# Kernel optimization log

Hardware: AMD Instinct MI355X
Metric: run time of the kernel (lower is better)

## Reference

```python
import jax, jax.numpy as jnp
import numpy as np

N = 50000      # nodes
R = 4          # relations
EMB = 128      # embedding size
H = 4          # heads
S = EMB // H   # per-head size (32)
E = 400000     # total edges (100k per relation)


def setup_inputs() -> dict:
    key = jax.random.key(0)
    ks = jax.random.split(key, 8)
    def u(k, shape, sc):
        return jax.random.uniform(k, shape, jnp.float32, -sc, sc)
    sS = 1.0 / np.sqrt(S)
    sE = 1.0 / np.sqrt(EMB)
    return {
        "x": jax.random.normal(ks[0], (N, EMB), jnp.float32),
        "tokeys": u(ks[1], (R, H, S, S), sS),
        "toqueries": u(ks[2], (R, H, S, S), sS),
        "tovals": u(ks[3], (R, H, S, S), sS),
        "unify": u(ks[4], (R, EMB, EMB), sE),
        "edge_sub": jax.random.randint(ks[5], (E,), 0, N),
        "edge_pred": jax.random.randint(ks[6], (E,), 0, R),
        "edge_obj": jax.random.randint(ks[7], (E,), 0, N),
    }


def reference(x, tokeys, toqueries, tovals, unify, edge_sub, edge_pred, edge_obj):
    n, e = x.shape
    r, h, s, _ = tokeys.shape
    xh = x.reshape(n, h, s)  # x is broadcast (expanded) across relations in the original

    # per-relation, per-head projections: [r, n, h, s]
    keys = jnp.einsum('rhij,nhj->rnhi', tokeys, xh)
    queries = jnp.einsum('rhij,nhj->rnhi', toqueries, xh)
    values = jnp.einsum('rhij,nhj->rnhi', tovals, xh)

    # gather per edge: key at subject, query at object (as in the torch code)
    skeys = keys[edge_pred, edge_sub]        # [E, h, s]
    squeries = queries[edge_pred, edge_obj]  # [E, h, s]
    dot = jnp.einsum('ehi,ehi->eh', skeys, squeries)  # [E, h]

    # segment softmax over rows of the (n*r, n*r) sparse matrix, per head
    row = edge_sub + edge_pred * n  # [E]
    num_seg = n * r
    seg_max = jax.ops.segment_max(dot, row, num_segments=num_seg)  # [n*r, h]
    ex = jnp.exp(dot - seg_max[row])
    seg_sum = jax.ops.segment_sum(ex, row, num_segments=num_seg)
    att = ex / seg_sum[row]  # [E, h]

    # sparse batched matmul: out[row] += att * values[col]  (util.batchmm)
    vals_g = values[edge_pred, edge_obj]          # [E, h, s]
    msg = att[:, :, None] * vals_g                # [E, h, s]
    agg = jax.ops.segment_sum(msg, row, num_segments=num_seg)  # [n*r, h, s]

    out = agg.reshape(r, n, e).transpose(1, 0, 2)  # [n, r, e] (h*s merged = e)
    out = jnp.einsum('rij,nrj->nri', unify, out)   # per-relation unify matmul
    return jax.nn.relu(out.sum(axis=1))            # SumUnify: relu(sum over relations)
```

## Files before the change

kernel.cpp:

```cpp
#include <hip/hip_runtime.h>

constexpr int N_NODES = 50000;
constexpr int N_REL   = 4;
constexpr int EMBD    = 128;
constexpr int N_HEAD  = 4;
constexpr int HS      = 32;
constexpr int N_EDGE  = 400000;
constexpr int N_ROWS  = N_REL * N_NODES;

typedef __attribute__((ext_vector_type(8))) short bf16x8;
typedef __attribute__((ext_vector_type(4))) float f32x4;
typedef unsigned short ushort_t;
typedef unsigned int   uint_t;

__device__ __forceinline__ ushort_t f2b(float f) {
    unsigned int u = __float_as_uint(f);
    u += 0x7FFF + ((u >> 16) & 1);
    return (ushort_t)(u >> 16);
}
__device__ __forceinline__ float lo_bf(uint_t u) {
    return __uint_as_float(u << 16);
}
__device__ __forceinline__ float hi_bf(uint_t u) {
    return __uint_as_float(u & 0xFFFF0000u);
}

__global__ __launch_bounds__(256) void prep_kernel(
    const float* __restrict__ x,
    const float* __restrict__ tk, const float* __restrict__ tq,
    const float* __restrict__ tv, const float* __restrict__ un,
    ushort_t* __restrict__ XB, int* __restrict__ HIST,
    ushort_t* __restrict__ Ct, ushort_t* __restrict__ Mb)
{
    int idx = blockIdx.x * 256 + threadIdx.x;
    if (idx < N_NODES * EMBD) {
        XB[idx] = f2b(x[idx]);
        if (idx < N_ROWS) HIST[idx] = 0;
    } else {
        int jj = idx - N_NODES * EMBD;
        if (jj < 16384) {
            int a = jj & 31, b = (jj >> 5) & 31, rh = jj >> 10;
            const float* tks = tk + rh * 1024;
            const float* tqs = tq + rh * 1024;
            float acc = 0.f;
            #pragma unroll
            for (int s = 0; s < 32; s++) acc += tks[s * 32 + a] * tqs[s * 32 + b];
            Ct[jj] = f2b(acc);
        } else {
            int j  = jj - 16384;
            int jc = j & 127, i = (j >> 7) & 127, r = j >> 14;
            int h = jc >> 5, k = jc & 31;
            const float* us  = un + ((size_t)(r * 128 + i)) * 128 + h * 32;
            const float* tvs = tv + (r * 4 + h) * 1024 + k;
            float acc = 0.f;
            #pragma unroll
            for (int s = 0; s < 32; s++) acc += us[s] * tvs[s * 32];
            Mb[j] = f2b(acc);
        }
    }
}

__global__ __launch_bounds__(512) void proj_mfma(
    const ushort_t* __restrict__ XB, const ushort_t* __restrict__ Ct,
    ushort_t* __restrict__ KT)
{
    __shared__ ushort_t xs[128 * 136];

    const int t    = threadIdx.x;
    const int lane = t & 63;
    const int w    = t >> 6;
    const int n0   = blockIdx.x * 128;

    {
        const uint4* x4 = (const uint4*)(XB + (size_t)n0 * 128);
        for (int idx = t; idx < 128 * 16; idx += 512) {
            int nn = idx >> 4, c = idx & 15;
            uint4 v = make_uint4(0, 0, 0, 0);
            if (n0 + nn < N_NODES) v = x4[idx];
            *(uint4*)&xs[nn * 136 + c * 8] = v;
        }
    }
    __syncthreads();

    const int row  = lane & 15;
    const int kg   = lane >> 4;
    const int rgrp = lane >> 4;

    #pragma unroll 1
    for (int r = 0; r < N_REL; r++) {
        f32x4 acc[8];
        #pragma unroll
        for (int f = 0; f < 8; f++) {
            const int h = f >> 1;
            bf16x8 a = *(const bf16x8*)&xs[(w * 16 + row) * 136 + h * 32 + kg * 8];
            const ushort_t* bp = Ct + (((r * 4 + h) * 32 + (f & 1) * 16 + row) * 32) + kg * 8;
            bf16x8 b = *(const bf16x8*)bp;
            acc[f] = __builtin_amdgcn_mfma_f32_16x16x32_bf16(
                         a, b, (f32x4){0.f, 0.f, 0.f, 0.f}, 0, 0, 0);
        }
        #pragma unroll
        for (int f = 0; f < 8; f++) {
            #pragma unroll
            for (int reg = 0; reg < 4; reg++) {
                int n = n0 + w * 16 + rgrp * 4 + reg;
                if (n < N_NODES)
                    KT[((size_t)r * N_NODES + n) * 128 + f * 16 + row] = f2b(acc[f][reg]);
            }
        }
    }
}

__global__ __launch_bounds__(256) void hist_kernel(
    const int* __restrict__ esub, const int* __restrict__ epred, int* __restrict__ HIST)
{
    int e = blockIdx.x * 256 + threadIdx.x;
    if (e < N_EDGE) atomicAdd(&HIST[epred[e] * N_NODES + esub[e]], 1);
}

__global__ __launch_bounds__(256) void scan_p1(
    const int* __restrict__ HIST, int* __restrict__ SUMS)
{
    int b = blockIdx.x, t = threadIdx.x;
    int base = b * 1024 + t * 4;
    int s = 0;
    #pragma unroll
    for (int k = 0; k < 4; k++) if (base + k < N_ROWS) s += HIST[base + k];
    __shared__ int red[256];
    red[t] = s; __syncthreads();
    for (int st = 128; st > 0; st >>= 1) {
        if (t < st) red[t] += red[t + st];
        __syncthreads();
    }
    if (t == 0) SUMS[b] = red[0];
}

__global__ __launch_bounds__(256) void scan_p2(
    const int* __restrict__ SUMS, int* __restrict__ SOFF, int* __restrict__ OFFS)
{
    int t = threadIdx.x;
    __shared__ int sh[256];
    int o = (t < 196) ? SUMS[t] : 0;
    sh[t] = o; __syncthreads();
    for (int st = 1; st < 256; st <<= 1) {
        int v = (t >= st) ? sh[t - st] : 0;
        __syncthreads();
        sh[t] += v;
        __syncthreads();
    }
    if (t < 196) SOFF[t] = sh[t] - o;
    if (t == 0)  OFFS[N_ROWS] = sh[255];
}

__global__ __launch_bounds__(256) void scan_p3(
    const int* __restrict__ HIST, const int* __restrict__ SOFF,
    int* __restrict__ OFFS, int* __restrict__ CURSOR)
{
    int b = blockIdx.x, t = threadIdx.x;
    int base = b * 1024 + t * 4;
    int v[4], tot = 0;
    #pragma unroll
    for (int k = 0; k < 4; k++) {
        v[k] = (base + k < N_ROWS) ? HIST[base + k] : 0;
        tot += v[k];
    }
    __shared__ int sh[256];
    sh[t] = tot; __syncthreads();
    for (int st = 1; st < 256; st <<= 1) {
        int q = (t >= st) ? sh[t - st] : 0;
        __syncthreads();
        sh[t] += q;
        __syncthreads();
    }
    int run = SOFF[b] + (sh[t] - tot);
    #pragma unroll
    for (int k = 0; k < 4; k++) {
        if (base + k < N_ROWS) { OFFS[base + k] = run; CURSOR[base + k] = run; run += v[k]; }
    }
}

__global__ __launch_bounds__(256) void scatter_kernel(
    const int* __restrict__ esub, const int* __restrict__ epred, const int* __restrict__ eobj,
    int* __restrict__ CURSOR, int* __restrict__ OBJS)
{
    int e = blockIdx.x * 256 + threadIdx.x;
    if (e < N_EDGE) {
        int row = epred[e] * N_NODES + esub[e];
        int pos = atomicAdd(&CURSOR[row], 1);
        OBJS[pos] = eobj[e];
    }
}

__global__ __launch_bounds__(256) void agg_fused(
    const int* __restrict__ OFFS, const int* __restrict__ OBJS,
    const uint_t* __restrict__ KT64, const uint_t* __restrict__ XB64,
    uint_t* __restrict__ AGG64)
{
    const int t    = threadIdx.x;
    const int lane = t & 63;
    const int row0 = (blockIdx.x * 4 + (t >> 6)) * 4;

    int off[5];
    #pragma unroll
    for (int q = 0; q < 5; q++) off[q] = OFFS[row0 + q];

    float klo[4], khi[4], aclo[4], achi[4], seg[4];
    int   it[4];
    #pragma unroll
    for (int q = 0; q < 4; q++) {
        it[q] = off[q];
        aclo[q] = 0.f; achi[q] = 0.f; seg[q] = 0.f;
        klo[q] = 0.f;  khi[q] = 0.f;
        if (off[q] < off[q + 1]) {
            uint_t ku = KT64[(unsigned)(row0 + q) * 64u + lane];
            klo[q] = lo_bf(ku); khi[q] = hi_bf(ku);
        }
    }

    while (it[0] < off[1] || it[1] < off[2] || it[2] < off[3] || it[3] < off[4]) {
        uint_t xu[4];
        bool   d[4];
        #pragma unroll
        for (int q = 0; q < 4; q++) {
            d[q]  = it[q] < off[q + 1];
            xu[q] = 0;
            if (d[q]) xu[q] = XB64[(unsigned)OBJS[it[q]] * 64u + lane];
        }
        float p[4];
        #pragma unroll
        for (int q = 0; q < 4; q++)
            p[q] = klo[q] * lo_bf(xu[q]) + khi[q] * hi_bf(xu[q]);
        #pragma unroll
        for (int m = 1; m < 16; m <<= 1) {
            #pragma unroll
            for (int q = 0; q < 4; q++) p[q] += __shfl_xor(p[q], m, 64);
        }
        #pragma unroll
        for (int q = 0; q < 4; q++) {
            if (d[q]) {
                float ex = __expf(p[q]);
                aclo[q] += ex * lo_bf(xu[q]);
                achi[q] += ex * hi_bf(xu[q]);
                seg[q]  += ex;
                it[q]++;
            }
        }
    }

    #pragma unroll
    for (int q = 0; q < 4; q++) {
        uint_t o = 0u;
        if (off[q] < off[q + 1]) {
            float inv = 1.0f / seg[q];
            o = (uint_t)f2b(aclo[q] * inv) | ((uint_t)f2b(achi[q] * inv) << 16);
        }
        AGG64[(unsigned)(row0 + q) * 64u + lane] = o;
    }
}

__global__ __launch_bounds__(256) void unify_mfma(
    const ushort_t* __restrict__ AGG,
    const ushort_t* __restrict__ Ub, float* __restrict__ out)
{
    __shared__ ushort_t As[64 * 136];
    __shared__ ushort_t Bs[128 * 136];

    const int t    = threadIdx.x;
    const int lane = t & 63;
    const int w    = t >> 6;
    const int n0   = blockIdx.x * 64;

    f32x4 acc[8];
    #pragma unroll
    for (int f = 0; f < 8; f++) acc[f] = (f32x4){0.f, 0.f, 0.f, 0.f};

    for (int r = 0; r < N_REL; r++) {
        __syncthreads();

        {
            const uint4* a4 = (const uint4*)(AGG + ((size_t)r * N_NODES + n0) * 128);
            for (int idx = t; idx < 64 * 16; idx += 256) {
                int nn = idx >> 4, c = idx & 15;
                uint4 v = make_uint4(0, 0, 0, 0);
                if (n0 + nn < N_NODES) v = a4[idx];
                *(uint4*)&As[nn * 136 + c * 8] = v;
            }
        }
        {
            const uint4* u4 = (const uint4*)(Ub + (size_t)r * 128 * 128);
            for (int idx = t; idx < 128 * 16; idx += 256) {
                int i = idx >> 4, c = idx & 15;
                *(uint4*)&Bs[i * 136 + c * 8] = u4[idx];
            }
        }
        __syncthreads();

        const int row = lane & 15;
        const int kg  = lane >> 4;
        #pragma unroll
        for (int ks = 0; ks < 4; ks++) {
            const int kofs = ks * 32 + kg * 8;
            bf16x8 a = *(const bf16x8*)&As[(w * 16 + row) * 136 + kofs];
            #pragma unroll
            for (int f = 0; f < 8; f++) {
                bf16x8 b = *(const bf16x8*)&Bs[(f * 16 + row) * 136 + kofs];
                acc[f] = __builtin_amdgcn_mfma_f32_16x16x32_bf16(a, b, acc[f], 0, 0, 0);
            }
        }
    }

    const int col  = lane & 15;
    const int rgrp = lane >> 4;
    #pragma unroll
    for (int f = 0; f < 8; f++) {
        #pragma unroll
        for (int reg = 0; reg < 4; reg++) {
            int n = n0 + w * 16 + rgrp * 4 + reg;
            if (n < N_NODES)
                out[(size_t)n * 128 + f * 16 + col] = fmaxf(acc[f][reg], 0.f);
        }
    }
}

extern "C" void kernel_launch(void* const* d_in, const int* in_sizes, int n_in,
                              void* d_out, int out_size, void* d_ws, size_t ws_size,
                              hipStream_t stream)
{
    const float* x  = (const float*)d_in[0];
    const float* tk = (const float*)d_in[1];
    const float* tq = (const float*)d_in[2];
    const float* tv = (const float*)d_in[3];
    const float* un = (const float*)d_in[4];
    const int* esub  = (const int*)d_in[5];
    const int* epred = (const int*)d_in[6];
    const int* eobj  = (const int*)d_in[7];
    float* out = (float*)d_out;

    char* ws = (char*)d_ws;
    ushort_t* KT  = (ushort_t*)(ws);
    ushort_t* XB  = (ushort_t*)(ws + 51200000);
    ushort_t* AGG = (ushort_t*)(ws + 64000000);
    int*      HIST= (int*)     (ws + 115200000);
    int*      SUMS= (int*)     (ws + 116000000);
    int*      SOFF= (int*)     (ws + 116004096);
    int*      OFFS= (int*)     (ws + 116008192);
    int*      OBJS= (int*)     (ws + 116816000);
    ushort_t* Mb  = (ushort_t*)(ws + 118416000);
    ushort_t* Ct  = (ushort_t*)(ws + 118547072);

    prep_kernel<<<(N_NODES * EMBD + 81920) / 256, 256, 0, stream>>>(
        x, tk, tq, tv, un, XB, HIST, Ct, Mb);

    hist_kernel<<<(N_EDGE + 255) / 256, 256, 0, stream>>>(esub, epred, HIST);
    scan_p1<<<196, 256, 0, stream>>>(HIST, SUMS);
    scan_p2<<<1, 256, 0, stream>>>(SUMS, SOFF, OFFS);
    scan_p3<<<196, 256, 0, stream>>>(HIST, SOFF, OFFS, HIST);
    scatter_kernel<<<(N_EDGE + 255) / 256, 256, 0, stream>>>(esub, epred, eobj, HIST, OBJS);

    proj_mfma<<<(N_NODES + 127) / 128, 512, 0, stream>>>(XB, Ct, KT);

    agg_fused<<<N_ROWS / 16, 256, 0, stream>>>(OFFS, OBJS,
                                               (const uint_t*)KT, (const uint_t*)XB,
                                               (uint_t*)AGG);

    unify_mfma<<<(N_NODES + 63) / 64, 256, 0, stream>>>(AGG, Mb, out);
}
```

Measured before the change: 174.1 us.

## Bin rows by degree so aggregation warps process similar-length segments

Adds a degree histogram per scan block, a global bin scan and a scatter that builds a row permutation sorted by (clamped) degree. The aggregation kernel then assigns four degree-similar rows per wavefront via this permutation, reducing divergence where the loop runs to the longest of four rows. Dot-product shuffles are also moved inside the per-row active branch to skip reductions for finished rows. Costs two extra small kernels and indirect, less coalesced row access for K and output writes.

```diff
diff --git a/kernel.cpp b/kernel.cpp
--- a/kernel.cpp
+++ b/kernel.cpp
@@ -7,6 +7,8 @@
 constexpr int HS      = 32;
 constexpr int N_EDGE  = 400000;
 constexpr int N_ROWS  = N_REL * N_NODES;
+constexpr int N_SBLK  = 196;
+constexpr int N_BIN   = 16;
 
 typedef __attribute__((ext_vector_type(8))) short bf16x8;
 typedef __attribute__((ext_vector_type(4))) float f32x4;
@@ -139,7 +141,7 @@
 {
     int t = threadIdx.x;
     __shared__ int sh[256];
-    int o = (t < 196) ? SUMS[t] : 0;
+    int o = (t < N_SBLK) ? SUMS[t] : 0;
     sh[t] = o; __syncthreads();
     for (int st = 1; st < 256; st <<= 1) {
         int v = (t >= st) ? sh[t - st] : 0;
@@ -147,13 +149,13 @@
         sh[t] += v;
         __syncthreads();
     }
-    if (t < 196) SOFF[t] = sh[t] - o;
+    if (t < N_SBLK) SOFF[t] = sh[t] - o;
     if (t == 0)  OFFS[N_ROWS] = sh[255];
 }
 
 __global__ __launch_bounds__(256) void scan_p3(
     const int* __restrict__ HIST, const int* __restrict__ SOFF,
-    int* __restrict__ OFFS, int* __restrict__ CURSOR)
+    int* __restrict__ OFFS, int* __restrict__ CURSOR, int* __restrict__ BH)
 {
     int b = blockIdx.x, t = threadIdx.x;
     int base = b * 1024 + t * 4;
@@ -164,7 +166,13 @@
         tot += v[k];
     }
     __shared__ int sh[256];
+    __shared__ int bh[N_BIN];
+    if (t < N_BIN) bh[t] = 0;
     sh[t] = tot; __syncthreads();
+    #pragma unroll
+    for (int k = 0; k < 4; k++) {
+        if (base + k < N_ROWS) atomicAdd(&bh[min(v[k], 15)], 1);
+    }
     for (int st = 1; st < 256; st <<= 1) {
         int q = (t >= st) ? sh[t - st] : 0;
         __syncthreads();
@@ -176,6 +184,8 @@
     for (int k = 0; k < 4; k++) {
         if (base + k < N_ROWS) { OFFS[base + k] = run; CURSOR[base + k] = run; run += v[k]; }
     }
+    __syncthreads();
+    if (t < N_BIN) BH[b * N_BIN + t] = bh[t];
 }
 
 __global__ __launch_bounds__(256) void scatter_kernel(
@@ -190,54 +200,101 @@
     }
 }
 
+__global__ __launch_bounds__(256) void bin_scan(
+    const int* __restrict__ BH, int* __restrict__ BOFF)
+{
+    constexpr int TOT = N_SBLK * N_BIN;
+    __shared__ int vals[TOT];
+    __shared__ int part[256];
+    int t = threadIdx.x;
+    for (int i = t; i < TOT; i += 256) {
+        int bin = i / N_SBLK, blk = i % N_SBLK;
+        vals[i] = BH[blk * N_BIN + bin];
+    }
+    __syncthreads();
+    int c0 = t * 13;
+    int s = 0;
+    for (int k = 0; k < 13; k++) { int i = c0 + k; if (i < TOT) s += vals[i]; }
+    part[t] = s; __syncthreads();
+    for (int st = 1; st < 256; st <<= 1) {
+        int v = (t >= st) ? part[t - st] : 0;
+        __syncthreads();
+        part[t] += v;
+        __syncthreads();
+    }
+    int run = (t > 0) ? part[t - 1] : 0;
+    for (int k = 0; k < 13; k++) {
+        int i = c0 + k;
+        if (i < TOT) {
+            int bin = i / N_SBLK, blk = i % N_SBLK;
+            int v = vals[i];
+            BOFF[blk * N_BIN + bin] = run;
+            run += v;
+        }
+    }
+}
+
+__global__ __launch_bounds__(256) void bin_scatter(
+    const int* __restrict__ OFFS, const int* __restrict__ BOFF, int* __restrict__ ROWIDX)
+{
+    __shared__ int cur[N_BIN];
+    int b = blockIdx.x, t = threadIdx.x;
+    if (t < N_BIN) cur[t] = BOFF[b * N_BIN + t];
+    __syncthreads();
+    int base = b * 1024 + t * 4;
+    #pragma unroll
+    for (int k = 0; k < 4; k++) {
+        int i = base + k;
+        if (i < N_ROWS) {
+            int deg = OFFS[i + 1] - OFFS[i];
+            int pos = atomicAdd(&cur[min(deg, 15)], 1);
+            ROWIDX[pos] = i;
+        }
+    }
+}
+
 __global__ __launch_bounds__(256) void agg_fused(
-    const int* __restrict__ OFFS, const int* __restrict__ OBJS,
+    const int* __restrict__ ROWIDX, const int* __restrict__ OFFS,
+    const int* __restrict__ OBJS,
     const uint_t* __restrict__ KT64, const uint_t* __restrict__ XB64,
     uint_t* __restrict__ AGG64)
 {
     const int t    = threadIdx.x;
     const int lane = t & 63;
-    const int row0 = (blockIdx.x * 4 + (t >> 6)) * 4;
-
-    int off[5];
-    #pragma unroll
-    for (int q = 0; q < 5; q++) off[q] = OFFS[row0 + q];
-
+    const int s0   = (blockIdx.x * 4 + (t >> 6)) * 4;
+
+    int rows[4], bq[4], eq[4], it[4];
     float klo[4], khi[4], aclo[4], achi[4], seg[4];
-    int   it[4];
     #pragma unroll
     for (int q = 0; q < 4; q++) {
-        it[q] = off[q];
+        rows[q] = ROWIDX[s0 + q];
+        bq[q] = OFFS[rows[q]];
+        eq[q] = OFFS[rows[q] + 1];
+        it[q] = bq[q];
         aclo[q] = 0.f; achi[q] = 0.f; seg[q] = 0.f;
         klo[q] = 0.f;  khi[q] = 0.f;
-        if (off[q] < off[q + 1]) {
-            uint_t ku = KT64[(unsigned)(row0 + q) * 64u + lane];
+        if (bq[q] < eq[q]) {
+            uint_t ku = KT64[(unsigned)rows[q] * 64u + lane];
             klo[q] = lo_bf(ku); khi[q] = hi_bf(ku);
         }
     }
 
-    while (it[0] < off[1] || it[1] < off[2] || it[2] < off[3] || it[3] < off[4]) {
+    while (it[0] < eq[0] || it[1] < eq[1] || it[2] < eq[2] || it[3] < eq[3]) {
         uint_t xu[4];
         bool   d[4];
         #pragma unroll
         for (int q = 0; q < 4; q++) {
-            d[q]  = it[q] < off[q + 1];
+            d[q]  = it[q] < eq[q];
             xu[q] = 0;
             if (d[q]) xu[q] = XB64[(unsigned)OBJS[it[q]] * 64u + lane];
         }
-        float p[4];
-        #pragma unroll
-        for (int q = 0; q < 4; q++)
-            p[q] = klo[q] * lo_bf(xu[q]) + khi[q] * hi_bf(xu[q]);
-        #pragma unroll
-        for (int m = 1; m < 16; m <<= 1) {
-            #pragma unroll
-            for (int q = 0; q < 4; q++) p[q] += __shfl_xor(p[q], m, 64);
-        }
         #pragma unroll
         for (int q = 0; q < 4; q++) {
             if (d[q]) {
-                float ex = __expf(p[q]);
+                float p = klo[q] * lo_bf(xu[q]) + khi[q] * hi_bf(xu[q]);
+                #pragma unroll
+                for (int m = 1; m < 16; m <<= 1) p += __shfl_xor(p, m, 64);
+                float ex = __expf(p);
                 aclo[q] += ex * lo_bf(xu[q]);
                 achi[q] += ex * hi_bf(xu[q]);
                 seg[q]  += ex;
@@ -249,11 +306,11 @@
     #pragma unroll
     for (int q = 0; q < 4; q++) {
         uint_t o = 0u;
-        if (off[q] < off[q + 1]) {
+        if (bq[q] < eq[q]) {
             float inv = 1.0f / seg[q];
             o = (uint_t)f2b(aclo[q] * inv) | ((uint_t)f2b(achi[q] * inv) << 16);
         }
-        AGG64[(unsigned)(row0 + q) * 64u + lane] = o;
+        AGG64[(unsigned)rows[q] * 64u + lane] = o;
     }
 }
 
@@ -336,29 +393,35 @@
     float* out = (float*)d_out;
 
     char* ws = (char*)d_ws;
-    ushort_t* KT  = (ushort_t*)(ws);
-    ushort_t* XB  = (ushort_t*)(ws + 51200000);
-    ushort_t* AGG = (ushort_t*)(ws + 64000000);
-    int*      HIST= (int*)     (ws + 115200000);
-    int*      SUMS= (int*)     (ws + 116000000);
-    int*      SOFF= (int*)     (ws + 116004096);
-    int*      OFFS= (int*)     (ws + 116008192);
-    int*      OBJS= (int*)     (ws + 116816000);
-    ushort_t* Mb  = (ushort_t*)(ws + 118416000);
-    ushort_t* Ct  = (ushort_t*)(ws + 118547072);
+    ushort_t* KT    = (ushort_t*)(ws);
+    ushort_t* XB    = (ushort_t*)(ws + 51200000);
+    ushort_t* AGG   = (ushort_t*)(ws + 64000000);
+    int*      HIST  = (int*)     (ws + 115200000);
+    int*      SUMS  = (int*)     (ws + 116000000);
+    int*      SOFF  = (int*)     (ws + 116004096);
+    int*      OFFS  = (int*)     (ws + 116008192);
+    int*      OBJS  = (int*)     (ws + 116816000);
+    ushort_t* Mb    = (ushort_t*)(ws + 118416000);
+    ushort_t* Ct    = (ushort_t*)(ws + 118547072);
+    int*      ROWIDX= (int*)     (ws + 118579840);
+    int*      BH    = (int*)     (ws + 119379840);
+    int*      BOFF  = (int*)     (ws + 119396224);
 
     prep_kernel<<<(N_NODES * EMBD + 81920) / 256, 256, 0, stream>>>(
         x, tk, tq, tv, un, XB, HIST, Ct, Mb);
 
     hist_kernel<<<(N_EDGE + 255) / 256, 256, 0, stream>>>(esub, epred, HIST);
-    scan_p1<<<196, 256, 0, stream>>>(HIST, SUMS);
+    scan_p1<<<N_SBLK, 256, 0, stream>>>(HIST, SUMS);
     scan_p2<<<1, 256, 0, stream>>>(SUMS, SOFF, OFFS);
-    scan_p3<<<196, 256, 0, stream>>>(HIST, SOFF, OFFS, HIST);
+    scan_p3<<<N_SBLK, 256, 0, stream>>>(HIST, SOFF, OFFS, HIST, BH);
     scatter_kernel<<<(N_EDGE + 255) / 256, 256, 0, stream>>>(esub, epred, eobj, HIST, OBJS);
 
+    bin_scan<<<1, 256, 0, stream>>>(BH, BOFF);
+    bin_scatter<<<N_SBLK, 256, 0, stream>>>(OFFS, BOFF, ROWIDX);
+
     proj_mfma<<<(N_NODES + 127) / 128, 512, 0, stream>>>(XB, Ct, KT);
 
-    agg_fused<<<N_ROWS / 16, 256, 0, stream>>>(OFFS, OBJS,
+    agg_fused<<<N_ROWS / 16, 256, 0, stream>>>(ROWIDX, OFFS, OBJS,
                                                (const uint_t*)KT, (const uint_t*)XB,
                                                (uint_t*)AGG);
 
```

Result: slower. 197.7 us (+13.6%).

## Remap aggregation to half-wave per row with 8-byte loads and two-edge unroll

Applied to the files above, without the earlier changes.

The aggregation kernel now assigns each CSR row to 32 lanes instead of running four rows per wave in lockstep, with each lane loading 4 bf16 values via uint2. The inner loop handles two edges per iteration to expose more independent gathers, and the head reduction shrinks to 3 shuffle steps over 8 lanes. Two rows share a wave, so there is less divergence from rows of uneven length than with four, and the launch uses twice as many blocks. It also pulls the scan block count into a named constant.

```diff
diff --git a/kernel.cpp b/kernel.cpp
--- a/kernel.cpp
+++ b/kernel.cpp
@@ -7,6 +7,7 @@
 constexpr int HS      = 32;
 constexpr int N_EDGE  = 400000;
 constexpr int N_ROWS  = N_REL * N_NODES;
+constexpr int N_SBLK  = 196;
 
 typedef __attribute__((ext_vector_type(8))) short bf16x8;
 typedef __attribute__((ext_vector_type(4))) float f32x4;
@@ -139,7 +140,7 @@
 {
     int t = threadIdx.x;
     __shared__ int sh[256];
-    int o = (t < 196) ? SUMS[t] : 0;
+    int o = (t < N_SBLK) ? SUMS[t] : 0;
     sh[t] = o; __syncthreads();
     for (int st = 1; st < 256; st <<= 1) {
         int v = (t >= st) ? sh[t - st] : 0;
@@ -147,7 +148,7 @@
         sh[t] += v;
         __syncthreads();
     }
-    if (t < 196) SOFF[t] = sh[t] - o;
+    if (t < N_SBLK) SOFF[t] = sh[t] - o;
     if (t == 0)  OFFS[N_ROWS] = sh[255];
 }
 
@@ -192,69 +193,55 @@
 
 __global__ __launch_bounds__(256) void agg_fused(
     const int* __restrict__ OFFS, const int* __restrict__ OBJS,
-    const uint_t* __restrict__ KT64, const uint_t* __restrict__ XB64,
-    uint_t* __restrict__ AGG64)
+    const uint2* __restrict__ KT128, const uint2* __restrict__ XB128,
+    uint2* __restrict__ AGG128)
 {
     const int t    = threadIdx.x;
     const int lane = t & 63;
-    const int row0 = (blockIdx.x * 4 + (t >> 6)) * 4;
-
-    int off[5];
-    #pragma unroll
-    for (int q = 0; q < 5; q++) off[q] = OFFS[row0 + q];
-
-    float klo[4], khi[4], aclo[4], achi[4], seg[4];
-    int   it[4];
-    #pragma unroll
-    for (int q = 0; q < 4; q++) {
-        it[q] = off[q];
-        aclo[q] = 0.f; achi[q] = 0.f; seg[q] = 0.f;
-        klo[q] = 0.f;  khi[q] = 0.f;
-        if (off[q] < off[q + 1]) {
-            uint_t ku = KT64[(unsigned)(row0 + q) * 64u + lane];
-            klo[q] = lo_bf(ku); khi[q] = hi_bf(ku);
-        }
-    }
-
-    while (it[0] < off[1] || it[1] < off[2] || it[2] < off[3] || it[3] < off[4]) {
-        uint_t xu[4];
-        bool   d[4];
-        #pragma unroll
-        for (int q = 0; q < 4; q++) {
-            d[q]  = it[q] < off[q + 1];
-            xu[q] = 0;
-            if (d[q]) xu[q] = XB64[(unsigned)OBJS[it[q]] * 64u + lane];
-        }
-        float p[4];
-        #pragma unroll
-        for (int q = 0; q < 4; q++)
-            p[q] = klo[q] * lo_bf(xu[q]) + khi[q] * hi_bf(xu[q]);
-        #pragma unroll
-        for (int m = 1; m < 16; m <<= 1) {
-            #pragma unroll
-            for (int q = 0; q < 4; q++) p[q] += __shfl_xor(p[q], m, 64);
-        }
-        #pragma unroll
-        for (int q = 0; q < 4; q++) {
-            if (d[q]) {
-                float ex = __expf(p[q]);
-                aclo[q] += ex * lo_bf(xu[q]);
-                achi[q] += ex * hi_bf(xu[q]);
-                seg[q]  += ex;
-                it[q]++;
-            }
-        }
-    }
-
-    #pragma unroll
-    for (int q = 0; q < 4; q++) {
-        uint_t o = 0u;
-        if (off[q] < off[q + 1]) {
-            float inv = 1.0f / seg[q];
-            o = (uint_t)f2b(aclo[q] * inv) | ((uint_t)f2b(achi[q] * inv) << 16);
-        }
-        AGG64[(unsigned)(row0 + q) * 64u + lane] = o;
-    }
+    const int l5   = lane & 31;
+    const int row  = (blockIdx.x * 4 + (t >> 6)) * 2 + (lane >> 5);
+
+    const int beg = OFFS[row], end = OFFS[row + 1];
+    const bool has = beg < end;
+
+    float k0 = 0.f, k1 = 0.f, k2 = 0.f, k3 = 0.f;
+    if (has) {
+        uint2 ku = KT128[(unsigned)row * 32u + l5];
+        k0 = lo_bf(ku.x); k1 = hi_bf(ku.x); k2 = lo_bf(ku.y); k3 = hi_bf(ku.y);
+    }
+
+    float a0 = 0.f, a1 = 0.f, a2 = 0.f, a3 = 0.f, seg = 0.f;
+    int it = beg;
+    while (__any(it < end)) {
+        const bool d0 = it < end;
+        const bool d1 = it + 1 < end;
+        uint2 xu0 = make_uint2(0u, 0u), xu1 = make_uint2(0u, 0u);
+        if (d0) xu0 = XB128[(unsigned)OBJS[it] * 32u + l5];
+        if (d1) xu1 = XB128[(unsigned)OBJS[it + 1] * 32u + l5];
+
+        float x00 = lo_bf(xu0.x), x01 = hi_bf(xu0.x), x02 = lo_bf(xu0.y), x03 = hi_bf(xu0.y);
+        float x10 = lo_bf(xu1.x), x11 = hi_bf(xu1.x), x12 = lo_bf(xu1.y), x13 = hi_bf(xu1.y);
+
+        float p0 = k0 * x00 + k1 * x01 + k2 * x02 + k3 * x03;
+        float p1 = k0 * x10 + k1 * x11 + k2 * x12 + k3 * x13;
+        p0 += __shfl_xor(p0, 1, 64); p1 += __shfl_xor(p1, 1, 64);
+        p0 += __shfl_xor(p0, 2, 64); p1 += __shfl_xor(p1, 2, 64);
+        p0 += __shfl_xor(p0, 4, 64); p1 += __shfl_xor(p1, 4, 64);
+        float ex0 = __expf(p0), ex1 = __expf(p1);
+
+        int adv = 0;
+        if (d0) { a0 += ex0 * x00; a1 += ex0 * x01; a2 += ex0 * x02; a3 += ex0 * x03; seg += ex0; adv = 1; }
+        if (d1) { a0 += ex1 * x10; a1 += ex1 * x11; a2 += ex1 * x12; a3 += ex1 * x13; seg += ex1; adv = 2; }
+        it += adv;
+    }
+
+    uint2 o = make_uint2(0u, 0u);
+    if (has) {
+        float inv = 1.0f / seg;
+        o.x = (uint_t)f2b(a0 * inv) | ((uint_t)f2b(a1 * inv) << 16);
+        o.y = (uint_t)f2b(a2 * inv) | ((uint_t)f2b(a3 * inv) << 16);
+    }
+    AGG128[(unsigned)row * 32u + l5] = o;
 }
 
 __global__ __launch_bounds__(256) void unify_mfma(
@@ -351,16 +338,16 @@
         x, tk, tq, tv, un, XB, HIST, Ct, Mb);
 
     hist_kernel<<<(N_EDGE + 255) / 256, 256, 0, stream>>>(esub, epred, HIST);
-    scan_p1<<<196, 256, 0, stream>>>(HIST, SUMS);
+    scan_p1<<<N_SBLK, 256, 0, stream>>>(HIST, SUMS);
     scan_p2<<<1, 256, 0, stream>>>(SUMS, SOFF, OFFS);
-    scan_p3<<<196, 256, 0, stream>>>(HIST, SOFF, OFFS, HIST);
+    scan_p3<<<N_SBLK, 256, 0, stream>>>(HIST, SOFF, OFFS, HIST);
     scatter_kernel<<<(N_EDGE + 255) / 256, 256, 0, stream>>>(esub, epred, eobj, HIST, OBJS);
 
     proj_mfma<<<(N_NODES + 127) / 128, 512, 0, stream>>>(XB, Ct, KT);
 
-    agg_fused<<<N_ROWS / 16, 256, 0, stream>>>(OFFS, OBJS,
-                                               (const uint_t*)KT, (const uint_t*)XB,
-                                               (uint_t*)AGG);
+    agg_fused<<<N_ROWS / 8, 256, 0, stream>>>(OFFS, OBJS,
+                                              (const uint2*)KT, (const uint2*)XB,
+                                              (uint2*)AGG);
 
     unify_mfma<<<(N_NODES + 63) / 64, 256, 0, stream>>>(AGG, Mb, out);
 }
```

Result: faster. 162.0 us (-6.9%).
